# Performance work log

Hardware: AMD Instinct MI355X
Metric: run time of the kernel (lower is better)

## Reference

```python
import jax, jax.numpy as jnp
import numpy as np


def _gcn_conv(x, W, b, src, dst, n_nodes):
    # PyG GCNConv with add_self_loops=True, edge_weight=None (implicit ones),
    # symmetric normalization: D^{-1/2} A_hat D^{-1/2} (X W) + b
    xw = x @ W                                    # [N, H]
    loop = jnp.arange(n_nodes, dtype=src.dtype)
    src_f = jnp.concatenate([src, loop])          # [E+N]
    dst_f = jnp.concatenate([dst, loop])          # [E+N]
    w = jnp.ones(src_f.shape[0], dtype=x.dtype)
    deg = jax.ops.segment_sum(w, dst_f, num_segments=n_nodes)  # in-degree incl. self-loop
    dinv = jnp.where(deg > 0, jax.lax.rsqrt(deg), 0.0)
    norm = dinv[src_f] * dinv[dst_f]              # [E+N]
    msgs = norm[:, None] * xw[src_f]              # [E+N, H]
    out = jax.ops.segment_sum(msgs, dst_f, num_segments=n_nodes)
    return out + b


def setup_inputs() -> dict:
    key = jax.random.key(0)
    k1, k2, k3, k4 = jax.random.split(key, 4)
    N, E, D, H = 100000, 1600000, 256, 128
    x = jax.random.normal(k1, (N, D), dtype=jnp.float32)
    edge_index = jax.random.randint(k2, (2, E), 0, N, dtype=jnp.int64)
    # Glorot-scaled weights
    W1 = jax.random.normal(k3, (D, H), dtype=jnp.float32) * np.sqrt(2.0 / (D + H))
    b1 = jnp.zeros((H,), dtype=jnp.float32)
    W2 = jax.random.normal(k4, (H, 1), dtype=jnp.float32) * np.sqrt(2.0 / (H + 1))
    b2 = jnp.zeros((1,), dtype=jnp.float32)
    return {"x": x, "edge_index": edge_index, "W1": W1, "b1": b1, "W2": W2, "b2": b2}


def reference(x, edge_index, W1, b1, W2, b2):
    n_nodes = x.shape[0]
    src, dst = edge_index[0], edge_index[1]
    h = _gcn_conv(x, W1, b1, src, dst, n_nodes)   # conv1
    h = jax.nn.relu(h)                            # relu; dropout is identity in eval mode
    out = _gcn_conv(h, W2, b2, src, dst, n_nodes) # conv2 -> [N, 1]
    return out.reshape(-1)                        # x.view(-1)
```

## Files before the change

### kernel.cpp

```cpp
#include <hip/hip_runtime.h>
#include <hip/hip_fp16.h>
#include <cstdint>
#include <cstddef>


#define ELLW 64
#define BSH 9
#define BNODES (1 << BSH)
#define BPAD 16
#define BCAP 12288

typedef _Float16 half8 __attribute__((ext_vector_type(8)));
typedef _Float16 half2t __attribute__((ext_vector_type(2)));
typedef float floatx4 __attribute__((ext_vector_type(4)));
typedef float floatv4 __attribute__((ext_vector_type(4)));
typedef int intv4 __attribute__((ext_vector_type(4)));
typedef unsigned int uintv4 __attribute__((ext_vector_type(4)));

__global__ __launch_bounds__(256) void prep_k(const float* __restrict__ W1,
                                              _Float16* __restrict__ wz,
                                              _Float16* __restrict__ z1h,
                                              float* __restrict__ z2w,
                                              int* __restrict__ cnt,
                                              int* __restrict__ gcur,
                                              int N, int NB) {
  int b = blockIdx.x, tid = threadIdx.x;
  if (b < 128) {
    int id = b * 256 + tid;
    int j = id & 7, lane = (id >> 3) & 63, nb = (id >> 9) & 7, kb = id >> 12;
    int k = kb * 32 + ((lane >> 4) << 3) + j;
    int n = nb * 16 + (lane & 15);
    wz[id] = (_Float16)W1[k * 128 + n];
  } else if (b == 128) {
    if (tid < 128) z1h[(size_t)N * 128 + tid] = (_Float16)0.f;
    if (tid == 0) { z2w[N] = 0.f; cnt[N] = 0; }
  } else {
    int i = (b - 129) * 256 + tid;
    if (i < NB * BPAD) gcur[i] = 0;
  }
}

__global__ __launch_bounds__(256) void stage_k(int kind, int fb, int g0,
                                               const float* __restrict__ X,
                                               const _Float16* __restrict__ wz,
                                               _Float16* __restrict__ z1h, int N,
                                               const int* __restrict__ src,
                                               const int* __restrict__ dst,
                                               int* __restrict__ gcur,
                                               int* __restrict__ barr,
                                               int* __restrict__ ell,
                                               int* __restrict__ cnt,
                                               int E, int NB) {
  __shared__ char lds_raw[16 * 1024];
  int tid = threadIdx.x;

  if ((int)blockIdx.x < fb) {
    if (kind == 0) {
      int* bc = (int*)lds_raw;
      int* bb = bc + 256;
      for (int i = tid; i < NB; i += 256) bc[i] = 0;
      __syncthreads();
      int base = ((int)blockIdx.x * 256 + tid) * 8;
      int dv[8], sv[8], rv[8], bkv[8];
      int ne = 0;
      if (base + 7 < E) {
        intv4 d0 = __builtin_nontemporal_load((const intv4*)(dst + base));
        intv4 d1 = __builtin_nontemporal_load((const intv4*)(dst + base + 4));
        intv4 s0 = __builtin_nontemporal_load((const intv4*)(src + base));
        intv4 s1 = __builtin_nontemporal_load((const intv4*)(src + base + 4));
        dv[0] = d0[0]; dv[1] = d0[1]; dv[2] = d0[2]; dv[3] = d0[3];
        dv[4] = d1[0]; dv[5] = d1[1]; dv[6] = d1[2]; dv[7] = d1[3];
        sv[0] = s0[0]; sv[1] = s0[1]; sv[2] = s0[2]; sv[3] = s0[3];
        sv[4] = s1[0]; sv[5] = s1[1]; sv[6] = s1[2]; sv[7] = s1[3];
        ne = 8;
      } else {
        for (int e = base; e < E && e < base + 8; ++e) {
          dv[ne] = dst[e]; sv[ne] = src[e]; ++ne;
        }
      }
      for (int i = 0; i < ne; ++i) {
        bkv[i] = dv[i] >> BSH;
        rv[i] = atomicAdd(&bc[bkv[i]], 1);
      }
      __syncthreads();
      for (int i = tid; i < NB; i += 256) {
        int cc = bc[i];
        bb[i] = cc ? atomicAdd(&gcur[i * BPAD], cc) : 0;
      }
      __syncthreads();
      for (int i = 0; i < ne; ++i) {
        int pos = bb[bkv[i]] + rv[i];
        if (pos < BCAP) {
          unsigned dl = (unsigned)(dv[i] & (BNODES - 1));
          barr[(size_t)bkv[i] * BCAP + pos] = (int)((dl << 23) | (unsigned)sv[i]);
        }
      }
    } else {
      int* cl = (int*)lds_raw;
      int bkt = (int)blockIdx.x;
      int lo = bkt << BSH;
      for (int i = tid; i < BNODES; i += 256) cl[i] = 0;
      __syncthreads();
      int cb = min(gcur[bkt * BPAD], BCAP);
      const int* seg = barr + (size_t)bkt * BCAP;
      for (int e = tid; e < cb; e += 256) {
        unsigned v = (unsigned)seg[e];
        int dl = (int)(v >> 23);
        int s = (int)(v & 0x7FFFFFu);
        int p = atomicAdd(&cl[dl], 1);
        if (p < ELLW) ell[(size_t)(lo + dl) * ELLW + p] = s;
      }
      __syncthreads();
      for (int i = tid; i < BNODES; i += 256) {
        int node = lo + i;
        if (node < N) cnt[node] = cl[i];
      }
    }
    return;
  }

  _Float16* Bl = (_Float16*)lds_raw;
  _Float16* Ol = (_Float16*)lds_raw;

  int wave = tid >> 6, lane = tid & 63;
  int m = lane & 15, q = lane >> 4;
  int row0 = (g0 + (int)blockIdx.x - fb) * 64;
  int row = row0 + wave * 16 + m;

  floatx4 acc[8];
#pragma unroll
  for (int nb = 0; nb < 8; ++nb) acc[nb] = (floatx4)(0.f);

  const uintv4* wsrc = (const uintv4*)wz;
  uintv4* bdst = (uintv4*)Bl;

#pragma unroll
  for (int ph = 0; ph < 4; ++ph) {
    if (ph) __syncthreads();
#pragma unroll
    for (int i = 0; i < 4; ++i) bdst[i * 256 + tid] = wsrc[ph * 1024 + i * 256 + tid];
    __syncthreads();
#pragma unroll
    for (int kk = 0; kk < 2; ++kk) {
      int kb = ph * 2 + kk;
      half8 a;
      if (row < N) {
        const floatv4* ap = (const floatv4*)(X + (size_t)row * 256 + kb * 32 + q * 8);
        floatv4 a0 = __builtin_nontemporal_load(ap);
        floatv4 a1 = __builtin_nontemporal_load(ap + 1);
        a[0] = (_Float16)a0[0]; a[1] = (_Float16)a0[1];
        a[2] = (_Float16)a0[2]; a[3] = (_Float16)a0[3];
        a[4] = (_Float16)a1[0]; a[5] = (_Float16)a1[1];
        a[6] = (_Float16)a1[2]; a[7] = (_Float16)a1[3];
      } else {
#pragma unroll
        for (int j = 0; j < 8; ++j) a[j] = (_Float16)0.f;
      }
#pragma unroll
      for (int nb = 0; nb < 8; ++nb) {
        half8 b = *(const half8*)(Bl + ((size_t)(kk * 8 + nb) * 64 + lane) * 8);
        acc[nb] = __builtin_amdgcn_mfma_f32_16x16x32_f16(a, b, acc[nb], 0, 0, 0);
      }
    }
  }
  __syncthreads();

#pragma unroll
  for (int nb = 0; nb < 8; ++nb) {
    int col = nb * 16 + m;
#pragma unroll
    for (int r = 0; r < 4; ++r) {
      int orow = wave * 16 + q * 4 + r;
      Ol[orow * 128 + col] = (_Float16)acc[nb][r];
    }
  }
  __syncthreads();

  const uintv4* osrc = (const uintv4*)Ol;
  uintv4* gdst = (uintv4*)(z1h + (size_t)row0 * 128);
#pragma unroll
  for (int i = 0; i < 4; ++i) {
    int idx = i * 256 + tid;
    int r = idx >> 4;
    if (row0 + r < N) gdst[idx] = osrc[idx];
  }
}

__global__ __launch_bounds__(256) void agg1_k(const _Float16* __restrict__ z1h,
                                              const int* __restrict__ cnt,
                                              const int* __restrict__ ell,
                                              const float* __restrict__ b1,
                                              const float* __restrict__ W2,
                                              float* __restrict__ z2w, int N) {
  int d = blockIdx.x * 4 + (threadIdx.x >> 6);
  int lane = threadIdx.x & 63;
  if (d >= N) return;
  int cd = cnt[d];
  int c = min(cd, ELLW);
  int raw = __builtin_nontemporal_load(ell + (size_t)d * ELLW + lane);
  int idx = (lane < c) ? raw : N;
  float wl = rsqrtf((float)(cnt[idx] + 1));
  float dd = rsqrtf((float)(cd + 1));

  half2t self = ((const half2t*)(z1h + (size_t)d * 128))[lane];
  float ax = dd * (float)self[0];
  float ay = dd * (float)self[1];

  int e = 0;
  for (; e + 16 <= c; e += 16) {
#pragma unroll
    for (int j = 0; j < 16; ++j) {
      int s = __builtin_amdgcn_readlane(idx, e + j);
      float w = __int_as_float(__builtin_amdgcn_readlane(__float_as_int(wl), e + j));
      half2t v = ((const half2t*)(z1h + (size_t)s * 128))[lane];
      ax = fmaf(w, (float)v[0], ax);
      ay = fmaf(w, (float)v[1], ay);
    }
  }
  int cpad = (c + 3) & ~3;
  for (; e < cpad; e += 4) {
#pragma unroll
    for (int j = 0; j < 4; ++j) {
      int s = __builtin_amdgcn_readlane(idx, e + j);
      float w = __int_as_float(__builtin_amdgcn_readlane(__float_as_int(wl), e + j));
      half2t v = ((const half2t*)(z1h + (size_t)s * 128))[lane];
      ax = fmaf(w, (float)v[0], ax);
      ay = fmaf(w, (float)v[1], ay);
    }
  }

  float2 bb = ((const float2*)b1)[lane];
  float hx = fmaxf(fmaf(dd, ax, bb.x), 0.f);
  float hy = fmaxf(fmaf(dd, ay, bb.y), 0.f);
  float2 w2 = ((const float2*)W2)[lane];
  float dot = hx * w2.x + hy * w2.y;
#pragma unroll
  for (int off = 32; off >= 1; off >>= 1) dot += __shfl_xor(dot, off, 64);
  if (lane == 0) z2w[d] = dd * dot;
}

__global__ __launch_bounds__(256) void agg2_k(const float* __restrict__ z2w,
                                              const int* __restrict__ cnt,
                                              const int* __restrict__ ell,
                                              const float* __restrict__ b2,
                                              float* __restrict__ out, int N) {
  int d = blockIdx.x * 4 + (threadIdx.x >> 6);
  int lane = threadIdx.x & 63;
  if (d >= N) return;
  int cd = cnt[d];
  int c = min(cd, ELLW);
  int raw = __builtin_nontemporal_load(ell + (size_t)d * ELLW + lane);
  int idx = (lane < c) ? raw : N;
  float v = z2w[idx];
#pragma unroll
  for (int off = 32; off >= 1; off >>= 1) v += __shfl_xor(v, off, 64);
  if (lane == 0) out[d] = rsqrtf((float)(cd + 1)) * (v + z2w[d]) + b2[0];
}

extern "C" void kernel_launch(void* const* d_in, const int* in_sizes, int n_in,
                              void* d_out, int out_size, void* d_ws, size_t ws_size,
                              hipStream_t stream) {
  (void)n_in; (void)out_size; (void)ws_size;
  const float* x = (const float*)d_in[0];
  const int* edge = (const int*)d_in[1];
  const float* W1 = (const float*)d_in[2];
  const float* b1 = (const float*)d_in[3];
  const float* W2 = (const float*)d_in[4];
  const float* b2 = (const float*)d_in[5];
  float* out = (float*)d_out;

  const int D = 256, H = 128;
  int N = in_sizes[0] / D;
  int E = in_sizes[1] / 2;
  const int* srcp = edge;
  const int* dstp = edge + E;
  int NB = (N + BNODES - 1) >> BSH;

  char* ws = (char*)d_ws;
  size_t off = 0;
  auto alloc = [&](size_t bytes) -> void* {
    void* p = ws + off;
    off += (bytes + 255) & ~(size_t)255;
    return p;
  };
  int* cnt        = (int*)alloc((size_t)(N + 1) * 4);
  float* z2w      = (float*)alloc((size_t)(N + 1) * 4);
  int* ell        = (int*)alloc((size_t)N * ELLW * 4);
  _Float16* wz    = (_Float16*)alloc((size_t)32768 * 2);
  _Float16* z1h   = (_Float16*)alloc((size_t)(N + 1) * H * 2);
  int* gcur       = (int*)alloc((size_t)NB * BPAD * 4);
  int* barr       = (int*)alloc((size_t)NB * BCAP * 4);

  int tiles = (N + 63) / 64;
  int gh = tiles / 2;
  int fbA = (E + 2047) / 2048;
  int fbB = NB;

  prep_k<<<dim3(129 + (NB * BPAD + 255) / 256), dim3(256), 0, stream>>>(
      W1, wz, z1h, z2w, cnt, gcur, N, NB);
  stage_k<<<dim3(fbA + gh), dim3(256), 0, stream>>>(0, fbA, 0, x, wz, z1h, N,
      srcp, dstp, gcur, barr, ell, cnt, E, NB);
  stage_k<<<dim3(fbB + (tiles - gh)), dim3(256), 0, stream>>>(1, fbB, gh, x, wz, z1h, N,
      srcp, dstp, gcur, barr, ell, cnt, E, NB);
  agg1_k<<<dim3((N + 3) / 4), dim3(256), 0, stream>>>(z1h, cnt, ell, b1, W2, z2w, N);
  agg2_k<<<dim3((N + 3) / 4), dim3(256), 0, stream>>>(z2w, cnt, ell, b2, out, N);
}
```

Baseline: 298.1 us.

## Prescale XW rows by source inverse-sqrt degree in bucket pass, simplify aggregation

After the bucket pass has computed per-node degrees, each z1h row is scaled by its own rsqrt(deg+1). The layer-1 aggregation then becomes a plain sum of neighbor rows, dropping the per-edge gather of neighbor degree counts, the weight readlane and the FMAs. To make this safe, all GEMM tiles now run in the first stage launch and the second launch only builds the ELL buckets, so z1h is complete before it is rescaled. The cost is an extra read-modify-write over z1h, one fp16 rounding of the scaled value, and a less balanced split of work between the two stage launches.

```diff
diff --git a/kernel.cpp b/kernel.cpp
--- a/kernel.cpp
+++ b/kernel.cpp
@@ -115,6 +115,16 @@
         int node = lo + i;
         if (node < N) cnt[node] = cl[i];
       }
+      int nrows = min(BNODES, N - lo);
+      for (int j = tid; j < nrows * 64; j += 256) {
+        int r = j >> 6;
+        float sc = rsqrtf((float)(cl[r] + 1));
+        half2t* p = (half2t*)(z1h + (size_t)(lo + r) * 128) + (j & 63);
+        half2t v = *p;
+        v[0] = (_Float16)((float)v[0] * sc);
+        v[1] = (_Float16)((float)v[1] * sc);
+        *p = v;
+      }
     }
     return;
   }
@@ -199,22 +209,22 @@
   int c = min(cd, ELLW);
   int raw = __builtin_nontemporal_load(ell + (size_t)d * ELLW + lane);
   int idx = (lane < c) ? raw : N;
-  float wl = rsqrtf((float)(cnt[idx] + 1));
   float dd = rsqrtf((float)(cd + 1));
 
-  half2t self = ((const half2t*)(z1h + (size_t)d * 128))[lane];
-  float ax = dd * (float)self[0];
-  float ay = dd * (float)self[1];
+  const char* zb = (const char*)z1h;
+  int lane4 = lane * 4;
+  half2t self = *(const half2t*)(zb + ((size_t)d << 8) + lane4);
+  float ax = (float)self[0];
+  float ay = (float)self[1];
 
   int e = 0;
   for (; e + 16 <= c; e += 16) {
 #pragma unroll
     for (int j = 0; j < 16; ++j) {
       int s = __builtin_amdgcn_readlane(idx, e + j);
-      float w = __int_as_float(__builtin_amdgcn_readlane(__float_as_int(wl), e + j));
-      half2t v = ((const half2t*)(z1h + (size_t)s * 128))[lane];
-      ax = fmaf(w, (float)v[0], ax);
-      ay = fmaf(w, (float)v[1], ay);
+      half2t v = *(const half2t*)(zb + ((size_t)s << 8) + lane4);
+      ax += (float)v[0];
+      ay += (float)v[1];
     }
   }
   int cpad = (c + 3) & ~3;
@@ -222,10 +232,9 @@
 #pragma unroll
     for (int j = 0; j < 4; ++j) {
       int s = __builtin_amdgcn_readlane(idx, e + j);
-      float w = __int_as_float(__builtin_amdgcn_readlane(__float_as_int(wl), e + j));
-      half2t v = ((const half2t*)(z1h + (size_t)s * 128))[lane];
-      ax = fmaf(w, (float)v[0], ax);
-      ay = fmaf(w, (float)v[1], ay);
+      half2t v = *(const half2t*)(zb + ((size_t)s << 8) + lane4);
+      ax += (float)v[0];
+      ay += (float)v[1];
     }
   }
 
@@ -292,15 +301,14 @@
   int* barr       = (int*)alloc((size_t)NB * BCAP * 4);
 
   int tiles = (N + 63) / 64;
-  int gh = tiles / 2;
   int fbA = (E + 2047) / 2048;
   int fbB = NB;
 
   prep_k<<<dim3(129 + (NB * BPAD + 255) / 256), dim3(256), 0, stream>>>(
       W1, wz, z1h, z2w, cnt, gcur, N, NB);
-  stage_k<<<dim3(fbA + gh), dim3(256), 0, stream>>>(0, fbA, 0, x, wz, z1h, N,
+  stage_k<<<dim3(fbA + tiles), dim3(256), 0, stream>>>(0, fbA, 0, x, wz, z1h, N,
       srcp, dstp, gcur, barr, ell, cnt, E, NB);
-  stage_k<<<dim3(fbB + (tiles - gh)), dim3(256), 0, stream>>>(1, fbB, gh, x, wz, z1h, N,
+  stage_k<<<dim3(fbB), dim3(256), 0, stream>>>(1, fbB, tiles, x, wz, z1h, N,
       srcp, dstp, gcur, barr, ell, cnt, E, NB);
   agg1_k<<<dim3((N + 3) / 4), dim3(256), 0, stream>>>(z1h, cnt, ell, b1, W2, z2w, N);
   agg2_k<<<dim3((N + 3) / 4), dim3(256), 0, stream>>>(z2w, cnt, ell, b2, out, N);
```

Result: slower. 330.3 us (+10.8%).

## Vectorize agg1 gather with 16-byte half8 loads and move all GEMM tiles to first stage

Applied to the files above, without the earlier changes.

The layer-1 aggregation now has each quarter-wave load a full neighbor row using 16-byte half8 loads. Each wave processes 8 neighbors per iteration, two per 16-lane group, and reduces the partial sums across groups with shuffles. The self-loop is folded into lane 0 of the neighbor list, so the ELL capacity drops to 63 real neighbors. The GEMM tiles are also moved entirely into the first stage launch, overlapping with edge bucketing, leaving the second launch for ELL build only. This aims to cut per-edge instruction count and improve memory-level parallelism in the gather, but it changes the overflow behaviour for nodes with 64 or more neighbors.

```diff
diff --git a/kernel.cpp b/kernel.cpp
--- a/kernel.cpp
+++ b/kernel.cpp
@@ -4,7 +4,7 @@
 #include <cstddef>
 
 
-#define ELLW 64
+#define ELLCAP 63
 #define BSH 9
 #define BNODES (1 << BSH)
 #define BPAD 16
@@ -108,7 +108,7 @@
         int dl = (int)(v >> 23);
         int s = (int)(v & 0x7FFFFFu);
         int p = atomicAdd(&cl[dl], 1);
-        if (p < ELLW) ell[(size_t)(lo + dl) * ELLW + p] = s;
+        if (p < ELLCAP) ell[(size_t)(lo + dl) * 64 + p] = s;
       }
       __syncthreads();
       for (int i = tid; i < BNODES; i += 256) {
@@ -196,46 +196,53 @@
   int lane = threadIdx.x & 63;
   if (d >= N) return;
   int cd = cnt[d];
-  int c = min(cd, ELLW);
-  int raw = __builtin_nontemporal_load(ell + (size_t)d * ELLW + lane);
-  int idx = (lane < c) ? raw : N;
+  int c = min(cd, ELLCAP);
+  int ct = c + 1;
+  int raw = ell[(size_t)d * 64 + lane];
+  int up = __shfl_up(raw, 1, 64);
+  int idx = (lane == 0) ? d : ((lane < ct) ? up : N);
   float wl = rsqrtf((float)(cnt[idx] + 1));
   float dd = rsqrtf((float)(cd + 1));
 
-  half2t self = ((const half2t*)(z1h + (size_t)d * 128))[lane];
-  float ax = dd * (float)self[0];
-  float ay = dd * (float)self[1];
-
-  int e = 0;
-  for (; e + 16 <= c; e += 16) {
-#pragma unroll
-    for (int j = 0; j < 16; ++j) {
-      int s = __builtin_amdgcn_readlane(idx, e + j);
-      float w = __int_as_float(__builtin_amdgcn_readlane(__float_as_int(wl), e + j));
-      half2t v = ((const half2t*)(z1h + (size_t)s * 128))[lane];
-      ax = fmaf(w, (float)v[0], ax);
-      ay = fmaf(w, (float)v[1], ay);
-    }
-  }
-  int cpad = (c + 3) & ~3;
-  for (; e < cpad; e += 4) {
-#pragma unroll
-    for (int j = 0; j < 4; ++j) {
-      int s = __builtin_amdgcn_readlane(idx, e + j);
-      float w = __int_as_float(__builtin_amdgcn_readlane(__float_as_int(wl), e + j));
-      half2t v = ((const half2t*)(z1h + (size_t)s * 128))[lane];
-      ax = fmaf(w, (float)v[0], ax);
-      ay = fmaf(w, (float)v[1], ay);
-    }
-  }
-
-  float2 bb = ((const float2*)b1)[lane];
-  float hx = fmaxf(fmaf(dd, ax, bb.x), 0.f);
-  float hy = fmaxf(fmaf(dd, ay, bb.y), 0.f);
-  float2 w2 = ((const float2*)W2)[lane];
-  float dot = hx * w2.x + hy * w2.y;
-#pragma unroll
-  for (int off = 32; off >= 1; off >>= 1) dot += __shfl_xor(dot, off, 64);
+  int g = lane >> 4;
+  int a8 = (lane & 15) * 8;
+  float acc[8];
+#pragma unroll
+  for (int k = 0; k < 8; ++k) acc[k] = 0.f;
+
+  for (int t = 0; t < ct; t += 8) {
+    int s0 = __shfl(idx, t + g, 64);
+    float w0 = __shfl(wl, t + g, 64);
+    int s1 = __shfl(idx, t + 4 + g, 64);
+    float w1 = __shfl(wl, t + 4 + g, 64);
+    half8 v0 = *(const half8*)(z1h + (size_t)s0 * 128 + a8);
+    half8 v1 = *(const half8*)(z1h + (size_t)s1 * 128 + a8);
+#pragma unroll
+    for (int k = 0; k < 8; ++k) acc[k] = fmaf(w0, (float)v0[k], acc[k]);
+#pragma unroll
+    for (int k = 0; k < 8; ++k) acc[k] = fmaf(w1, (float)v1[k], acc[k]);
+  }
+
+#pragma unroll
+  for (int k = 0; k < 8; ++k) {
+    acc[k] += __shfl_xor(acc[k], 16, 64);
+    acc[k] += __shfl_xor(acc[k], 32, 64);
+  }
+
+  float4 bA = *(const float4*)(b1 + a8);
+  float4 bB = *(const float4*)(b1 + a8 + 4);
+  float4 wA = *(const float4*)(W2 + a8);
+  float4 wB = *(const float4*)(W2 + a8 + 4);
+  float dot = fmaxf(fmaf(dd, acc[0], bA.x), 0.f) * wA.x
+            + fmaxf(fmaf(dd, acc[1], bA.y), 0.f) * wA.y
+            + fmaxf(fmaf(dd, acc[2], bA.z), 0.f) * wA.z
+            + fmaxf(fmaf(dd, acc[3], bA.w), 0.f) * wA.w
+            + fmaxf(fmaf(dd, acc[4], bB.x), 0.f) * wB.x
+            + fmaxf(fmaf(dd, acc[5], bB.y), 0.f) * wB.y
+            + fmaxf(fmaf(dd, acc[6], bB.z), 0.f) * wB.z
+            + fmaxf(fmaf(dd, acc[7], bB.w), 0.f) * wB.w;
+#pragma unroll
+  for (int off = 8; off >= 1; off >>= 1) dot += __shfl_xor(dot, off, 64);
   if (lane == 0) z2w[d] = dd * dot;
 }
 
@@ -248,8 +255,8 @@
   int lane = threadIdx.x & 63;
   if (d >= N) return;
   int cd = cnt[d];
-  int c = min(cd, ELLW);
-  int raw = __builtin_nontemporal_load(ell + (size_t)d * ELLW + lane);
+  int c = min(cd, ELLCAP);
+  int raw = ell[(size_t)d * 64 + lane];
   int idx = (lane < c) ? raw : N;
   float v = z2w[idx];
 #pragma unroll
@@ -285,22 +292,21 @@
   };
   int* cnt        = (int*)alloc((size_t)(N + 1) * 4);
   float* z2w      = (float*)alloc((size_t)(N + 1) * 4);
-  int* ell        = (int*)alloc((size_t)N * ELLW * 4);
+  int* ell        = (int*)alloc((size_t)N * 64 * 4);
   _Float16* wz    = (_Float16*)alloc((size_t)32768 * 2);
   _Float16* z1h   = (_Float16*)alloc((size_t)(N + 1) * H * 2);
   int* gcur       = (int*)alloc((size_t)NB * BPAD * 4);
   int* barr       = (int*)alloc((size_t)NB * BCAP * 4);
 
   int tiles = (N + 63) / 64;
-  int gh = tiles / 2;
   int fbA = (E + 2047) / 2048;
   int fbB = NB;
 
   prep_k<<<dim3(129 + (NB * BPAD + 255) / 256), dim3(256), 0, stream>>>(
       W1, wz, z1h, z2w, cnt, gcur, N, NB);
-  stage_k<<<dim3(fbA + gh), dim3(256), 0, stream>>>(0, fbA, 0, x, wz, z1h, N,
+  stage_k<<<dim3(fbA + tiles), dim3(256), 0, stream>>>(0, fbA, 0, x, wz, z1h, N,
       srcp, dstp, gcur, barr, ell, cnt, E, NB);
-  stage_k<<<dim3(fbB + (tiles - gh)), dim3(256), 0, stream>>>(1, fbB, gh, x, wz, z1h, N,
+  stage_k<<<dim3(fbB), dim3(256), 0, stream>>>(1, fbB, tiles, x, wz, z1h, N,
       srcp, dstp, gcur, barr, ell, cnt, E, NB);
   agg1_k<<<dim3((N + 3) / 4), dim3(256), 0, stream>>>(z1h, cnt, ell, b1, W2, z2w, N);
   agg2_k<<<dim3((N + 3) / 4), dim3(256), 0, stream>>>(z2w, cnt, ell, b2, out, N);
```

Result: faster. 292.0 us (-2.0%).
